# Optimization experiments

Hardware: AMD Instinct MI355X
Metric: run time of the kernel (lower is better)

## Reference

```python
import jax, jax.numpy as jnp
import numpy as np

N_NODES = 50000
N_EDGES = 800000
N_GRAPHS = 512
IN_CH, HID_CH, OUT_CH, N_CLASSES = 128, 64, 64, 10


def gcn_conv(x, src, dst, ew, W, b, n_nodes):
    """PyG GCNConv: add self-loops (weight 1), symmetric normalization, x @ W, scatter-add at dst, + bias."""
    xw = x @ W  # [N, out]
    loop = jnp.arange(n_nodes, dtype=src.dtype)
    src_f = jnp.concatenate([src, loop])
    dst_f = jnp.concatenate([dst, loop])
    ew_f = jnp.concatenate([ew, jnp.ones((n_nodes,), dtype=ew.dtype)])
    deg = jax.ops.segment_sum(ew_f, dst_f, num_segments=n_nodes)  # [N]
    dinv = jnp.where(deg > 0, jax.lax.rsqrt(deg), 0.0)
    norm = dinv[src_f] * ew_f * dinv[dst_f]  # [E+N]
    msg = norm[:, None] * xw[src_f]  # gather + scale
    out = jax.ops.segment_sum(msg, dst_f, num_segments=n_nodes)  # scatter-add
    return out + b


def setup_inputs() -> dict:
    key = jax.random.key(0)
    ks = jax.random.split(key, 12)
    x = jax.random.normal(ks[0], (N_NODES, IN_CH), dtype=jnp.float32)
    edge_index = jax.random.randint(ks[1], (2, N_EDGES), 0, N_NODES, dtype=jnp.int64)
    edge_attr = jax.random.uniform(ks[2], (N_EDGES,), dtype=jnp.float32)
    batch = jnp.sort(jax.random.randint(ks[3], (N_NODES,), 0, N_GRAPHS, dtype=jnp.int64))
    def glorot(k, shape):
        lim = np.sqrt(6.0 / (shape[0] + shape[1]))
        return jax.random.uniform(k, shape, jnp.float32, -lim, lim)
    W1 = glorot(ks[4], (IN_CH, HID_CH))
    b1 = jnp.zeros((HID_CH,), jnp.float32)
    W2 = glorot(ks[5], (HID_CH, OUT_CH))
    b2 = jnp.zeros((OUT_CH,), jnp.float32)
    LW1 = glorot(ks[6], (OUT_CH, 32))
    Lb1 = jnp.zeros((32,), jnp.float32)
    LW2 = glorot(ks[7], (32, N_CLASSES))
    Lb2 = jnp.zeros((N_CLASSES,), jnp.float32)
    return {"x": x, "edge_index": edge_index, "edge_attr": edge_attr, "batch": batch,
            "W1": W1, "b1": b1, "W2": W2, "b2": b2,
            "LW1": LW1, "Lb1": Lb1, "LW2": LW2, "Lb2": Lb2}


def reference(x, edge_index, edge_attr, batch, W1, b1, W2, b2, LW1, Lb1, LW2, Lb2):
    src, dst = edge_index[0], edge_index[1]
    h = gcn_conv(x, src, dst, edge_attr, W1, b1, N_NODES)
    h = jax.nn.relu(h)
    h = gcn_conv(h, src, dst, edge_attr, W2, b2, N_NODES)
    # global mean pool over graphs
    sums = jax.ops.segment_sum(h, batch, num_segments=N_GRAPHS)  # [G, OUT]
    cnt = jax.ops.segment_sum(jnp.ones((N_NODES,), h.dtype), batch, num_segments=N_GRAPHS)
    pooled = sums / jnp.maximum(cnt, 1.0)[:, None]
    # head (dropout treated as identity for deterministic reference)
    h1 = pooled @ LW1 + Lb1
    return h1 @ LW2 + Lb2
```

## Files before the change

### kernel.cpp

```cpp
#include <hip/hip_runtime.h>
#include <hip/hip_bf16.h>

static constexpr int NN = 50000;
static constexpr int NE = 800000;
static constexpr int NG = 512;
static constexpr int NB = 196;

__device__ __forceinline__ float bfu(ushort u) {
    return __uint_as_float((unsigned)u << 16);
}
__device__ __forceinline__ ushort fbf(float f) {
    return __hip_bfloat16_raw(__float2bfloat16(f)).x;
}


__global__ void zero_kernel(float* __restrict__ p, int n) {
    int i = blockIdx.x * blockDim.x + threadIdx.x;
    if (i < n) p[i] = 0.f;
}

__global__ void hist64_kernel(const int* __restrict__ dst, const float* __restrict__ ew,
                              unsigned long long* __restrict__ h, int* __restrict__ rank) {
    int e = blockIdx.x * blockDim.x + threadIdx.x;
    if (e >= NE) return;
    int d = dst[e];
    unsigned int fx = __float2uint_rn(ew[e] * 1048576.0f);
    unsigned long long pack = (1ULL << 40) | (unsigned long long)fx;
    unsigned long long old = atomicAdd(&h[d], pack);
    rank[e] = (int)(old >> 40);
}

__global__ __launch_bounds__(256) void dinv_scanA_kernel(const unsigned long long* __restrict__ h,
                                                         float* __restrict__ dinv,
                                                         int* __restrict__ partial) {
    int i = blockIdx.x * 256 + threadIdx.x;
    int cnt = 0;
    if (i < NN) {
        unsigned long long v = h[i];
        cnt = (int)(v >> 40);
        float deg = (float)(v & ((1ULL << 40) - 1)) * (1.0f / 1048576.0f) + 1.0f;
        dinv[i] = 1.0f / sqrtf(deg);
    }
    __shared__ int wsum[4];
    int lane = threadIdx.x & 63, wid = threadIdx.x >> 6;
    int v = cnt;
#pragma unroll
    for (int off = 32; off > 0; off >>= 1) v += __shfl_down(v, (unsigned)off, 64);
    if (lane == 0) wsum[wid] = v;
    __syncthreads();
    if (threadIdx.x == 0) partial[blockIdx.x] = wsum[0] + wsum[1] + wsum[2] + wsum[3];
}

__device__ __forceinline__ int block_scan_inclusive(int v, int* wtot) {
    int lane = threadIdx.x & 63, wid = threadIdx.x >> 6;
    int inc = v;
#pragma unroll
    for (int off = 1; off < 64; off <<= 1) {
        int n = __shfl_up(inc, (unsigned)off, 64);
        if (lane >= off) inc += n;
    }
    if (lane == 63) wtot[wid] = inc;
    __syncthreads();
    int add = 0;
    for (int w = 0; w < wid; ++w) add += wtot[w];
    return inc + add;
}

__global__ __launch_bounds__(256) void scanB_kernel(const int* __restrict__ partial,
                                                    int* __restrict__ poff) {
    __shared__ int wtot[4];
    int t = threadIdx.x;
    int v = (t < NB) ? partial[t] : 0;
    int incl = block_scan_inclusive(v, wtot);
    if (t < NB) poff[t] = incl - v;
}

__global__ __launch_bounds__(256) void scanC_bounds_kernel(const unsigned long long* __restrict__ h,
                                                           const int* __restrict__ poff,
                                                           int* __restrict__ rowptr,
                                                           const int* __restrict__ batch,
                                                           int* __restrict__ gbeg,
                                                           int* __restrict__ gend) {
    __shared__ int wtot[4];
    int i = blockIdx.x * 256 + threadIdx.x;
    int v = (i < NN) ? (int)(h[i] >> 40) : 0;
    int incl = block_scan_inclusive(v, wtot);
    if (i < NN) {
        rowptr[i + 1] = poff[blockIdx.x] + incl;
        int g = batch[i];
        if (i == 0 || batch[i - 1] != g) gbeg[g] = i;
        if (i == NN - 1 || batch[i + 1] != g) gend[g] = i + 1;
    }
    if (i == 0) rowptr[0] = 0;
}

__global__ void scatter_kernel(const int* __restrict__ src, const int* __restrict__ dst,
                               const float* __restrict__ ew, const float* __restrict__ dinv,
                               const int* __restrict__ rowptr, const int* __restrict__ rank,
                               int2* __restrict__ epack) {
    int e = blockIdx.x * blockDim.x + threadIdx.x;
    if (e >= NE) return;
    int s = src[e], d = dst[e];
    int pos = rowptr[d] + rank[e];
    float coef = dinv[s] * ew[e];
    epack[pos] = make_int2(s, __float_as_int(coef));
}

template <int K, bool BF16IN>
__global__ __launch_bounds__(256) void gemm_kernel(const void* __restrict__ Xv,
                                                   const float* __restrict__ W,
                                                   ushort* __restrict__ out) {
    __shared__ float Xs[64][68];
    __shared__ float Ws[K][64];
    for (int i = threadIdx.x; i < K * 16; i += 256)
        ((float4*)Ws)[i] = ((const float4*)W)[i];
    int tx = threadIdx.x & 15, ty = threadIdx.x >> 4;
    int row0 = blockIdx.x * 64;
    float acc[4][4] = {};
    for (int kb = 0; kb < K; kb += 64) {
        __syncthreads();
        if constexpr (BF16IN) {
            const ushort* X = (const ushort*)Xv;
            for (int i = threadIdx.x; i < 512; i += 256) {
                int r = i >> 3, g = i & 7;
                int gr = row0 + r; if (gr >= NN) gr = NN - 1;
                uint4 v = *(const uint4*)(X + (long long)gr * K + kb + g * 8);
                float4 f0, f1;
                f0.x = __uint_as_float(v.x << 16); f0.y = __uint_as_float(v.x & 0xffff0000u);
                f0.z = __uint_as_float(v.y << 16); f0.w = __uint_as_float(v.y & 0xffff0000u);
                f1.x = __uint_as_float(v.z << 16); f1.y = __uint_as_float(v.z & 0xffff0000u);
                f1.z = __uint_as_float(v.w << 16); f1.w = __uint_as_float(v.w & 0xffff0000u);
                *(float4*)&Xs[r][g * 8] = f0;
                *(float4*)&Xs[r][g * 8 + 4] = f1;
            }
        } else {
            const float* X = (const float*)Xv;
            for (int i = threadIdx.x; i < 1024; i += 256) {
                int r = i >> 4, k4 = i & 15;
                int gr = row0 + r; if (gr >= NN) gr = NN - 1;
                float4 v = *(const float4*)(X + (long long)gr * K + kb + k4 * 4);
                *(float4*)&Xs[r][k4 * 4] = v;
            }
        }
        __syncthreads();
#pragma unroll 16
        for (int k = 0; k < 64; ++k) {
            float4 wv = *(const float4*)&Ws[kb + k][tx * 4];
            float x0 = Xs[ty * 4 + 0][k];
            float x1 = Xs[ty * 4 + 1][k];
            float x2 = Xs[ty * 4 + 2][k];
            float x3 = Xs[ty * 4 + 3][k];
            acc[0][0] = fmaf(x0, wv.x, acc[0][0]); acc[0][1] = fmaf(x0, wv.y, acc[0][1]);
            acc[0][2] = fmaf(x0, wv.z, acc[0][2]); acc[0][3] = fmaf(x0, wv.w, acc[0][3]);
            acc[1][0] = fmaf(x1, wv.x, acc[1][0]); acc[1][1] = fmaf(x1, wv.y, acc[1][1]);
            acc[1][2] = fmaf(x1, wv.z, acc[1][2]); acc[1][3] = fmaf(x1, wv.w, acc[1][3]);
            acc[2][0] = fmaf(x2, wv.x, acc[2][0]); acc[2][1] = fmaf(x2, wv.y, acc[2][1]);
            acc[2][2] = fmaf(x2, wv.z, acc[2][2]); acc[2][3] = fmaf(x2, wv.w, acc[2][3]);
            acc[3][0] = fmaf(x3, wv.x, acc[3][0]); acc[3][1] = fmaf(x3, wv.y, acc[3][1]);
            acc[3][2] = fmaf(x3, wv.z, acc[3][2]); acc[3][3] = fmaf(x3, wv.w, acc[3][3]);
        }
    }
#pragma unroll
    for (int j = 0; j < 4; ++j) {
        int r = row0 + ty * 4 + j;
        if (r < NN) {
            ushort4 sv;
            sv.x = fbf(acc[j][0]); sv.y = fbf(acc[j][1]);
            sv.z = fbf(acc[j][2]); sv.w = fbf(acc[j][3]);
            *(ushort4*)(out + (long long)r * 64 + tx * 4) = sv;
        }
    }
}

template <bool RELU, typename OutT>
__global__ __launch_bounds__(256) void agg_kernel(const ushort* __restrict__ xw,
                                                  const int* __restrict__ rowptr,
                                                  const int2* __restrict__ epack,
                                                  const float* __restrict__ dinv,
                                                  const float* __restrict__ bias,
                                                  OutT* __restrict__ out) {
    int node = blockIdx.x * 4 + (threadIdx.x >> 6);
    if (node >= NN) return;
    int lane = threadIdx.x & 63;
    int half = lane >> 5;
    int c2 = lane & 31;
    int beg = rowptr[node], end = rowptr[node + 1];
    float a0 = 0.f, a1 = 0.f, b0 = 0.f, b1 = 0.f;
    int j = beg + half;
    for (; j + 2 < end; j += 4) {
        int2 pa = epack[j];
        int2 pb = epack[j + 2];
        ushort2 ua = *(const ushort2*)(xw + pa.x * 64 + 2 * c2);
        ushort2 ub = *(const ushort2*)(xw + pb.x * 64 + 2 * c2);
        float wa = __int_as_float(pa.y);
        float wb = __int_as_float(pb.y);
        a0 = fmaf(wa, bfu(ua.x), a0);
        a1 = fmaf(wa, bfu(ua.y), a1);
        b0 = fmaf(wb, bfu(ub.x), b0);
        b1 = fmaf(wb, bfu(ub.y), b1);
    }
    if (j < end) {
        int2 pa = epack[j];
        ushort2 ua = *(const ushort2*)(xw + pa.x * 64 + 2 * c2);
        float wa = __int_as_float(pa.y);
        a0 = fmaf(wa, bfu(ua.x), a0);
        a1 = fmaf(wa, bfu(ua.y), a1);
    }
    a0 += b0; a1 += b1;
    a0 += __shfl_xor(a0, 32);
    a1 += __shfl_xor(a1, 32);
    if (half == 0) {
        float di = dinv[node];
        ushort2 us = *(const ushort2*)(xw + node * 64 + 2 * c2);
        float2 bv = *(const float2*)(bias + 2 * c2);
        float o0 = fmaf(di, a0, fmaf(di * di, bfu(us.x), bv.x));
        float o1 = fmaf(di, a1, fmaf(di * di, bfu(us.y), bv.y));
        if (RELU) { o0 = fmaxf(o0, 0.f); o1 = fmaxf(o1, 0.f); }
        if constexpr (sizeof(OutT) == 2) {
            ushort2 sv; sv.x = fbf(o0); sv.y = fbf(o1);
            *(ushort2*)((ushort*)out + node * 64 + 2 * c2) = sv;
        } else {
            float2 fv; fv.x = o0; fv.y = o1;
            *(float2*)((float*)out + node * 64 + 2 * c2) = fv;
        }
    }
}

__global__ __launch_bounds__(256) void poolhead_kernel(const float* __restrict__ h,
                                                       const int* __restrict__ gbeg,
                                                       const int* __restrict__ gend,
                                                       const float* __restrict__ LW1,
                                                       const float* __restrict__ Lb1,
                                                       const float* __restrict__ LW2,
                                                       const float* __restrict__ Lb2,
                                                       float* __restrict__ out) {
    __shared__ float pp[4][64];
    __shared__ float p[64];
    __shared__ float t1[32];
    int g = blockIdx.x, t = threadIdx.x;
    int lane = t & 63, wid = t >> 6;
    int b = gbeg[g], e = gend[g];
    float acc = 0.f;
    for (int i = b + wid; i < e; i += 4) acc += h[i * 64 + lane];
    pp[wid][lane] = acc;
    __syncthreads();
    if (t < 64) {
        float s = pp[0][t] + pp[1][t] + pp[2][t] + pp[3][t];
        p[t] = s / fmaxf((float)(e - b), 1.0f);
    }
    __syncthreads();
    if (t < 32) {
        float a = Lb1[t];
#pragma unroll
        for (int k = 0; k < 64; ++k) a = fmaf(p[k], LW1[k * 32 + t], a);
        t1[t] = a;
    }
    __syncthreads();
    if (t < 10) {
        float a = Lb2[t];
#pragma unroll
        for (int j = 0; j < 32; ++j) a = fmaf(t1[j], LW2[j * 10 + t], a);
        out[g * 10 + t] = a;
    }
}


extern "C" void kernel_launch(void* const* d_in, const int* in_sizes, int n_in,
                              void* d_out, int out_size, void* d_ws, size_t ws_size,
                              hipStream_t stream) {
    const float* x     = (const float*)d_in[0];
    const int*   ei    = (const int*)d_in[1];
    const float* ew    = (const float*)d_in[2];
    const int*   batch = (const int*)d_in[3];
    const float* W1    = (const float*)d_in[4];
    const float* b1    = (const float*)d_in[5];
    const float* W2    = (const float*)d_in[6];
    const float* b2    = (const float*)d_in[7];
    const float* LW1   = (const float*)d_in[8];
    const float* Lb1   = (const float*)d_in[9];
    const float* LW2   = (const float*)d_in[10];
    const float* Lb2   = (const float*)d_in[11];

    const int* src = ei;
    const int* dst = ei + NE;

    float* ws = (float*)d_ws;
    unsigned long long* h64 = (unsigned long long*)ws;
    int*   gbeg   = (int*)(ws + 100096);
    int*   gend   = (int*)(ws + 100608);
    float* dinv   = ws + 101120;
    int*   rowptr = (int*)(ws + 151168);
    int*   partial= (int*)(ws + 201216);
    int*   poff   = (int*)(ws + 201472);
    int2*  epack  = (int2*)(ws + 201728);
    ushort* xwA   = (ushort*)(ws + 1801728);
    ushort* h1    = (ushort*)(ws + 3401728);
    float* h2     = ws + 3401728;
    int*   rank   = (int*)(ws + 6601728);

    zero_kernel<<<(101120 + 255) / 256, 256, 0, stream>>>(ws, 101120);

    hist64_kernel<<<(NE + 255) / 256, 256, 0, stream>>>(dst, ew, h64, rank);
    dinv_scanA_kernel<<<NB, 256, 0, stream>>>(h64, dinv, partial);
    scanB_kernel<<<1, 256, 0, stream>>>(partial, poff);
    scanC_bounds_kernel<<<NB, 256, 0, stream>>>(h64, poff, rowptr, batch, gbeg, gend);
    scatter_kernel<<<(NE + 255) / 256, 256, 0, stream>>>(src, dst, ew, dinv, rowptr, rank, epack);

    gemm_kernel<128, false><<<(NN + 63) / 64, 256, 0, stream>>>(x, W1, xwA);
    agg_kernel<true, ushort><<<(NN + 3) / 4, 256, 0, stream>>>(xwA, rowptr, epack, dinv, b1, h1);

    gemm_kernel<64, true><<<(NN + 63) / 64, 256, 0, stream>>>(h1, W2, xwA);
    agg_kernel<false, float><<<(NN + 3) / 4, 256, 0, stream>>>(xwA, rowptr, epack, dinv, b2, h2);

    poolhead_kernel<<<NG, 256, 0, stream>>>(h2, gbeg, gend, LW1, Lb1, LW2, Lb2, (float*)d_out);
}
```

Before: 264.1 us.

## Fuse histogram with first GEMM, merge scan kernels, widen aggregation to ushort4

The degree histogram and the first X@W1 GEMM now run as one launch, with blocks split by blockIdx so the two independent phases can overlap. The single-block scanB pass is removed; each scanC block now sums the earlier partials itself. The aggregation kernel puts 4 edge groups of 16 lanes on each node and loads ushort4, and layer-2 output plus pooling now use bf16 instead of fp32. These changes cut launches and memory traffic, at the cost of some lost precision in h2, redundant partial sums in each block, and large shared-memory use in the histogram blocks, which may lower their occupancy.

```diff
diff --git a/kernel.cpp b/kernel.cpp
--- a/kernel.cpp
+++ b/kernel.cpp
@@ -5,6 +5,8 @@
 static constexpr int NE = 800000;
 static constexpr int NG = 512;
 static constexpr int NB = 196;
+static constexpr int HIST_BLOCKS = (NE + 255) / 256;
+static constexpr int GEMM_BLOCKS = (NN + 63) / 64;
 
 __device__ __forceinline__ float bfu(ushort u) {
     return __uint_as_float((unsigned)u << 16);
@@ -19,103 +21,14 @@
     if (i < n) p[i] = 0.f;
 }
 
-__global__ void hist64_kernel(const int* __restrict__ dst, const float* __restrict__ ew,
-                              unsigned long long* __restrict__ h, int* __restrict__ rank) {
-    int e = blockIdx.x * blockDim.x + threadIdx.x;
-    if (e >= NE) return;
-    int d = dst[e];
-    unsigned int fx = __float2uint_rn(ew[e] * 1048576.0f);
-    unsigned long long pack = (1ULL << 40) | (unsigned long long)fx;
-    unsigned long long old = atomicAdd(&h[d], pack);
-    rank[e] = (int)(old >> 40);
-}
-
-__global__ __launch_bounds__(256) void dinv_scanA_kernel(const unsigned long long* __restrict__ h,
-                                                         float* __restrict__ dinv,
-                                                         int* __restrict__ partial) {
-    int i = blockIdx.x * 256 + threadIdx.x;
-    int cnt = 0;
-    if (i < NN) {
-        unsigned long long v = h[i];
-        cnt = (int)(v >> 40);
-        float deg = (float)(v & ((1ULL << 40) - 1)) * (1.0f / 1048576.0f) + 1.0f;
-        dinv[i] = 1.0f / sqrtf(deg);
-    }
-    __shared__ int wsum[4];
-    int lane = threadIdx.x & 63, wid = threadIdx.x >> 6;
-    int v = cnt;
-#pragma unroll
-    for (int off = 32; off > 0; off >>= 1) v += __shfl_down(v, (unsigned)off, 64);
-    if (lane == 0) wsum[wid] = v;
-    __syncthreads();
-    if (threadIdx.x == 0) partial[blockIdx.x] = wsum[0] + wsum[1] + wsum[2] + wsum[3];
-}
-
-__device__ __forceinline__ int block_scan_inclusive(int v, int* wtot) {
-    int lane = threadIdx.x & 63, wid = threadIdx.x >> 6;
-    int inc = v;
-#pragma unroll
-    for (int off = 1; off < 64; off <<= 1) {
-        int n = __shfl_up(inc, (unsigned)off, 64);
-        if (lane >= off) inc += n;
-    }
-    if (lane == 63) wtot[wid] = inc;
-    __syncthreads();
-    int add = 0;
-    for (int w = 0; w < wid; ++w) add += wtot[w];
-    return inc + add;
-}
-
-__global__ __launch_bounds__(256) void scanB_kernel(const int* __restrict__ partial,
-                                                    int* __restrict__ poff) {
-    __shared__ int wtot[4];
-    int t = threadIdx.x;
-    int v = (t < NB) ? partial[t] : 0;
-    int incl = block_scan_inclusive(v, wtot);
-    if (t < NB) poff[t] = incl - v;
-}
-
-__global__ __launch_bounds__(256) void scanC_bounds_kernel(const unsigned long long* __restrict__ h,
-                                                           const int* __restrict__ poff,
-                                                           int* __restrict__ rowptr,
-                                                           const int* __restrict__ batch,
-                                                           int* __restrict__ gbeg,
-                                                           int* __restrict__ gend) {
-    __shared__ int wtot[4];
-    int i = blockIdx.x * 256 + threadIdx.x;
-    int v = (i < NN) ? (int)(h[i] >> 40) : 0;
-    int incl = block_scan_inclusive(v, wtot);
-    if (i < NN) {
-        rowptr[i + 1] = poff[blockIdx.x] + incl;
-        int g = batch[i];
-        if (i == 0 || batch[i - 1] != g) gbeg[g] = i;
-        if (i == NN - 1 || batch[i + 1] != g) gend[g] = i + 1;
-    }
-    if (i == 0) rowptr[0] = 0;
-}
-
-__global__ void scatter_kernel(const int* __restrict__ src, const int* __restrict__ dst,
-                               const float* __restrict__ ew, const float* __restrict__ dinv,
-                               const int* __restrict__ rowptr, const int* __restrict__ rank,
-                               int2* __restrict__ epack) {
-    int e = blockIdx.x * blockDim.x + threadIdx.x;
-    if (e >= NE) return;
-    int s = src[e], d = dst[e];
-    int pos = rowptr[d] + rank[e];
-    float coef = dinv[s] * ew[e];
-    epack[pos] = make_int2(s, __float_as_int(coef));
-}
-
 template <int K, bool BF16IN>
-__global__ __launch_bounds__(256) void gemm_kernel(const void* __restrict__ Xv,
-                                                   const float* __restrict__ W,
-                                                   ushort* __restrict__ out) {
-    __shared__ float Xs[64][68];
-    __shared__ float Ws[K][64];
+__device__ __forceinline__ void gemm_body(const void* __restrict__ Xv,
+                                          const float* __restrict__ W,
+                                          ushort* __restrict__ out,
+                                          int row0, float Xs[][68], float* Ws) {
     for (int i = threadIdx.x; i < K * 16; i += 256)
         ((float4*)Ws)[i] = ((const float4*)W)[i];
     int tx = threadIdx.x & 15, ty = threadIdx.x >> 4;
-    int row0 = blockIdx.x * 64;
     float acc[4][4] = {};
     for (int kb = 0; kb < K; kb += 64) {
         __syncthreads();
@@ -145,7 +58,7 @@
         __syncthreads();
 #pragma unroll 16
         for (int k = 0; k < 64; ++k) {
-            float4 wv = *(const float4*)&Ws[kb + k][tx * 4];
+            float4 wv = *(const float4*)&Ws[(kb + k) * 64 + tx * 4];
             float x0 = Xs[ty * 4 + 0][k];
             float x1 = Xs[ty * 4 + 1][k];
             float x2 = Xs[ty * 4 + 2][k];
@@ -172,61 +85,176 @@
     }
 }
 
-template <bool RELU, typename OutT>
+__global__ __launch_bounds__(256) void hist_gemm_kernel(const int* __restrict__ dst,
+                                                        const float* __restrict__ ew,
+                                                        unsigned long long* __restrict__ h,
+                                                        int* __restrict__ rank,
+                                                        const float* __restrict__ X,
+                                                        const float* __restrict__ W,
+                                                        ushort* __restrict__ out) {
+    __shared__ float Xs[64][68];
+    __shared__ float Ws[128 * 64];
+    if (blockIdx.x < HIST_BLOCKS) {
+        int e = blockIdx.x * 256 + threadIdx.x;
+        if (e >= NE) return;
+        int d = dst[e];
+        unsigned int fx = __float2uint_rn(ew[e] * 1048576.0f);
+        unsigned long long pack = (1ULL << 40) | (unsigned long long)fx;
+        unsigned long long old = atomicAdd(&h[d], pack);
+        rank[e] = (int)(old >> 40);
+        return;
+    }
+    gemm_body<128, false>(X, W, out, (blockIdx.x - HIST_BLOCKS) * 64, Xs, Ws);
+}
+
+template <int K, bool BF16IN>
+__global__ __launch_bounds__(256) void gemm_kernel(const void* __restrict__ Xv,
+                                                   const float* __restrict__ W,
+                                                   ushort* __restrict__ out) {
+    __shared__ float Xs[64][68];
+    __shared__ float Ws[K * 64];
+    gemm_body<K, BF16IN>(Xv, W, out, blockIdx.x * 64, Xs, Ws);
+}
+
+__global__ __launch_bounds__(256) void dinv_scanA_kernel(const unsigned long long* __restrict__ h,
+                                                         float* __restrict__ dinv,
+                                                         int* __restrict__ partial) {
+    int i = blockIdx.x * 256 + threadIdx.x;
+    int cnt = 0;
+    if (i < NN) {
+        unsigned long long v = h[i];
+        cnt = (int)(v >> 40);
+        float deg = (float)(v & ((1ULL << 40) - 1)) * (1.0f / 1048576.0f) + 1.0f;
+        dinv[i] = 1.0f / sqrtf(deg);
+    }
+    __shared__ int wsum[4];
+    int lane = threadIdx.x & 63, wid = threadIdx.x >> 6;
+    int v = cnt;
+#pragma unroll
+    for (int off = 32; off > 0; off >>= 1) v += __shfl_down(v, (unsigned)off, 64);
+    if (lane == 0) wsum[wid] = v;
+    __syncthreads();
+    if (threadIdx.x == 0) partial[blockIdx.x] = wsum[0] + wsum[1] + wsum[2] + wsum[3];
+}
+
+__device__ __forceinline__ int block_scan_inclusive(int v, int* wtot) {
+    int lane = threadIdx.x & 63, wid = threadIdx.x >> 6;
+    int inc = v;
+#pragma unroll
+    for (int off = 1; off < 64; off <<= 1) {
+        int n = __shfl_up(inc, (unsigned)off, 64);
+        if (lane >= off) inc += n;
+    }
+    if (lane == 63) wtot[wid] = inc;
+    __syncthreads();
+    int add = 0;
+    for (int w = 0; w < wid; ++w) add += wtot[w];
+    return inc + add;
+}
+
+__global__ __launch_bounds__(256) void scanC_bounds_kernel(const unsigned long long* __restrict__ h,
+                                                           const int* __restrict__ partial,
+                                                           int* __restrict__ rowptr,
+                                                           const int* __restrict__ batch,
+                                                           int* __restrict__ gbeg,
+                                                           int* __restrict__ gend) {
+    __shared__ int wtot[4];
+    __shared__ int poff_s;
+    int t = threadIdx.x;
+    if (t < 64) {
+        int s = 0;
+        for (int i = t; i < (int)blockIdx.x; i += 64) s += partial[i];
+#pragma unroll
+        for (int off = 32; off > 0; off >>= 1) s += __shfl_down(s, (unsigned)off, 64);
+        if (t == 0) poff_s = s;
+    }
+    int i = blockIdx.x * 256 + t;
+    int v = (i < NN) ? (int)(h[i] >> 40) : 0;
+    int incl = block_scan_inclusive(v, wtot);
+    if (i < NN) {
+        rowptr[i + 1] = poff_s + incl;
+        int g = batch[i];
+        if (i == 0 || batch[i - 1] != g) gbeg[g] = i;
+        if (i == NN - 1 || batch[i + 1] != g) gend[g] = i + 1;
+    }
+    if (i == 0) rowptr[0] = 0;
+}
+
+__global__ __launch_bounds__(256) void scatter_kernel(const int* __restrict__ src,
+                                                      const int* __restrict__ dst,
+                                                      const float* __restrict__ ew,
+                                                      const float* __restrict__ dinv,
+                                                      const int* __restrict__ rowptr,
+                                                      const int* __restrict__ rank,
+                                                      int2* __restrict__ epack) {
+    int e = blockIdx.x * blockDim.x + threadIdx.x;
+    if (e >= NE) return;
+    int s = src[e], d = dst[e];
+    int pos = rowptr[d] + rank[e];
+    float coef = dinv[s] * ew[e];
+    epack[pos] = make_int2(s, __float_as_int(coef));
+}
+
+template <bool RELU>
 __global__ __launch_bounds__(256) void agg_kernel(const ushort* __restrict__ xw,
                                                   const int* __restrict__ rowptr,
                                                   const int2* __restrict__ epack,
                                                   const float* __restrict__ dinv,
                                                   const float* __restrict__ bias,
-                                                  OutT* __restrict__ out) {
+                                                  ushort* __restrict__ out) {
     int node = blockIdx.x * 4 + (threadIdx.x >> 6);
     if (node >= NN) return;
     int lane = threadIdx.x & 63;
-    int half = lane >> 5;
-    int c2 = lane & 31;
+    int q = lane >> 4;
+    int l = lane & 15;
     int beg = rowptr[node], end = rowptr[node + 1];
-    float a0 = 0.f, a1 = 0.f, b0 = 0.f, b1 = 0.f;
-    int j = beg + half;
-    for (; j + 2 < end; j += 4) {
-        int2 pa = epack[j];
-        int2 pb = epack[j + 2];
-        ushort2 ua = *(const ushort2*)(xw + pa.x * 64 + 2 * c2);
-        ushort2 ub = *(const ushort2*)(xw + pb.x * 64 + 2 * c2);
-        float wa = __int_as_float(pa.y);
-        float wb = __int_as_float(pb.y);
-        a0 = fmaf(wa, bfu(ua.x), a0);
-        a1 = fmaf(wa, bfu(ua.y), a1);
-        b0 = fmaf(wb, bfu(ub.x), b0);
-        b1 = fmaf(wb, bfu(ub.y), b1);
+    float a0 = 0.f, a1 = 0.f, a2 = 0.f, a3 = 0.f;
+    float b0 = 0.f, b1 = 0.f, b2 = 0.f, b3 = 0.f;
+    int j = beg + q;
+    for (; j + 4 < end; j += 8) {
+        int2 pA = epack[j];
+        int2 pB = epack[j + 4];
+        ushort4 uA = *(const ushort4*)(xw + pA.x * 64 + 4 * l);
+        ushort4 uB = *(const ushort4*)(xw + pB.x * 64 + 4 * l);
+        float wA = __int_as_float(pA.y);
+        float wB = __int_as_float(pB.y);
+        a0 = fmaf(wA, bfu(uA.x), a0); a1 = fmaf(wA, bfu(uA.y), a1);
+        a2 = fmaf(wA, bfu(uA.z), a2); a3 = fmaf(wA, bfu(uA.w), a3);
+        b0 = fmaf(wB, bfu(uB.x), b0); b1 = fmaf(wB, bfu(uB.y), b1);
+        b2 = fmaf(wB, bfu(uB.z), b2); b3 = fmaf(wB, bfu(uB.w), b3);
     }
     if (j < end) {
-        int2 pa = epack[j];
-        ushort2 ua = *(const ushort2*)(xw + pa.x * 64 + 2 * c2);
-        float wa = __int_as_float(pa.y);
-        a0 = fmaf(wa, bfu(ua.x), a0);
-        a1 = fmaf(wa, bfu(ua.y), a1);
-    }
-    a0 += b0; a1 += b1;
-    a0 += __shfl_xor(a0, 32);
-    a1 += __shfl_xor(a1, 32);
-    if (half == 0) {
+        int2 pA = epack[j];
+        ushort4 uA = *(const ushort4*)(xw + pA.x * 64 + 4 * l);
+        float wA = __int_as_float(pA.y);
+        a0 = fmaf(wA, bfu(uA.x), a0); a1 = fmaf(wA, bfu(uA.y), a1);
+        a2 = fmaf(wA, bfu(uA.z), a2); a3 = fmaf(wA, bfu(uA.w), a3);
+    }
+    a0 += b0; a1 += b1; a2 += b2; a3 += b3;
+    a0 += __shfl_xor(a0, 16); a0 += __shfl_xor(a0, 32);
+    a1 += __shfl_xor(a1, 16); a1 += __shfl_xor(a1, 32);
+    a2 += __shfl_xor(a2, 16); a2 += __shfl_xor(a2, 32);
+    a3 += __shfl_xor(a3, 16); a3 += __shfl_xor(a3, 32);
+    if (q == 0) {
         float di = dinv[node];
-        ushort2 us = *(const ushort2*)(xw + node * 64 + 2 * c2);
-        float2 bv = *(const float2*)(bias + 2 * c2);
-        float o0 = fmaf(di, a0, fmaf(di * di, bfu(us.x), bv.x));
-        float o1 = fmaf(di, a1, fmaf(di * di, bfu(us.y), bv.y));
-        if (RELU) { o0 = fmaxf(o0, 0.f); o1 = fmaxf(o1, 0.f); }
-        if constexpr (sizeof(OutT) == 2) {
-            ushort2 sv; sv.x = fbf(o0); sv.y = fbf(o1);
-            *(ushort2*)((ushort*)out + node * 64 + 2 * c2) = sv;
-        } else {
-            float2 fv; fv.x = o0; fv.y = o1;
-            *(float2*)((float*)out + node * 64 + 2 * c2) = fv;
+        float d2 = di * di;
+        ushort4 us = *(const ushort4*)(xw + node * 64 + 4 * l);
+        float4 bv = *(const float4*)(bias + 4 * l);
+        float o0 = fmaf(di, a0, fmaf(d2, bfu(us.x), bv.x));
+        float o1 = fmaf(di, a1, fmaf(d2, bfu(us.y), bv.y));
+        float o2 = fmaf(di, a2, fmaf(d2, bfu(us.z), bv.z));
+        float o3 = fmaf(di, a3, fmaf(d2, bfu(us.w), bv.w));
+        if (RELU) {
+            o0 = fmaxf(o0, 0.f); o1 = fmaxf(o1, 0.f);
+            o2 = fmaxf(o2, 0.f); o3 = fmaxf(o3, 0.f);
         }
-    }
-}
-
-__global__ __launch_bounds__(256) void poolhead_kernel(const float* __restrict__ h,
+        ushort4 sv;
+        sv.x = fbf(o0); sv.y = fbf(o1); sv.z = fbf(o2); sv.w = fbf(o3);
+        *(ushort4*)(out + node * 64 + 4 * l) = sv;
+    }
+}
+
+__global__ __launch_bounds__(256) void poolhead_kernel(const ushort* __restrict__ h,
                                                        const int* __restrict__ gbeg,
                                                        const int* __restrict__ gend,
                                                        const float* __restrict__ LW1,
@@ -241,7 +269,7 @@
     int lane = t & 63, wid = t >> 6;
     int b = gbeg[g], e = gend[g];
     float acc = 0.f;
-    for (int i = b + wid; i < e; i += 4) acc += h[i * 64 + lane];
+    for (int i = b + wid; i < e; i += 4) acc += bfu(h[i * 64 + lane]);
     pp[wid][lane] = acc;
     __syncthreads();
     if (t < 64) {
@@ -291,26 +319,23 @@
     float* dinv   = ws + 101120;
     int*   rowptr = (int*)(ws + 151168);
     int*   partial= (int*)(ws + 201216);
-    int*   poff   = (int*)(ws + 201472);
-    int2*  epack  = (int2*)(ws + 201728);
-    ushort* xwA   = (ushort*)(ws + 1801728);
-    ushort* h1    = (ushort*)(ws + 3401728);
-    float* h2     = ws + 3401728;
-    int*   rank   = (int*)(ws + 6601728);
+    int2*  epack  = (int2*)(ws + 201472);
+    ushort* xwA   = (ushort*)(ws + 1801472);
+    ushort* h12   = (ushort*)(ws + 3401472);
+    int*   rank   = (int*)(ws + 5001472);
 
     zero_kernel<<<(101120 + 255) / 256, 256, 0, stream>>>(ws, 101120);
 
-    hist64_kernel<<<(NE + 255) / 256, 256, 0, stream>>>(dst, ew, h64, rank);
+    hist_gemm_kernel<<<HIST_BLOCKS + GEMM_BLOCKS, 256, 0, stream>>>(dst, ew, h64, rank,
+                                                                    x, W1, xwA);
     dinv_scanA_kernel<<<NB, 256, 0, stream>>>(h64, dinv, partial);
-    scanB_kernel<<<1, 256, 0, stream>>>(partial, poff);
-    scanC_bounds_kernel<<<NB, 256, 0, stream>>>(h64, poff, rowptr, batch, gbeg, gend);
+    scanC_bounds_kernel<<<NB, 256, 0, stream>>>(h64, partial, rowptr, batch, gbeg, gend);
     scatter_kernel<<<(NE + 255) / 256, 256, 0, stream>>>(src, dst, ew, dinv, rowptr, rank, epack);
 
-    gemm_kernel<128, false><<<(NN + 63) / 64, 256, 0, stream>>>(x, W1, xwA);
-    agg_kernel<true, ushort><<<(NN + 3) / 4, 256, 0, stream>>>(xwA, rowptr, epack, dinv, b1, h1);
-
-    gemm_kernel<64, true><<<(NN + 63) / 64, 256, 0, stream>>>(h1, W2, xwA);
-    agg_kernel<false, float><<<(NN + 3) / 4, 256, 0, stream>>>(xwA, rowptr, epack, dinv, b2, h2);
-
-    poolhead_kernel<<<NG, 256, 0, stream>>>(h2, gbeg, gend, LW1, Lb1, LW2, Lb2, (float*)d_out);
-}
+    agg_kernel<true><<<(NN + 3) / 4, 256, 0, stream>>>(xwA, rowptr, epack, dinv, b1, h12);
+
+    gemm_kernel<64, true><<<GEMM_BLOCKS, 256, 0, stream>>>(h12, W2, xwA);
+    agg_kernel<false><<<(NN + 3) / 4, 256, 0, stream>>>(xwA, rowptr, epack, dinv, b2, h12);
+
+    poolhead_kernel<<<NG, 256, 0, stream>>>(h12, gbeg, gend, LW1, Lb1, LW2, Lb2, (float*)d_out);
+}
```

New measurement: 244.5 us. 1.08x faster.
